# Optimization experiments

Measured on AMD Instinct MI355X. Metric: run time of the kernel, lower is better.

The kernel has to match this reference:

```python
import jax, jax.numpy as jnp
import numpy as np

K0 = 0.7978845608028654  # sqrt(2/pi)
C1 = 0.044715

def _gelu_tanh(x):
    # tanh-approx GELU, matching the Triton kernel's math
    return 0.5 * x * (1.0 + jnp.tanh(K0 * (x + C1 * x * x * x)))

def setup_inputs() -> dict:
    key = jax.random.key(0)
    k1, k2, k3 = jax.random.split(key, 3)
    B, C_in, H, W = 32, 64, 128, 128
    C_out, KH = 128, 3
    x = jax.random.normal(k1, (B, C_in, H, W), dtype=jnp.float32)
    weight = jax.random.normal(k2, (C_out, C_in, KH, KH), dtype=jnp.float32)
    bias = jax.random.normal(k3, (C_out,), dtype=jnp.float32)
    return {"x": x, "weight": weight, "bias": bias}

def reference(x, weight, bias):
    # Valid conv2d, stride 1 (NCHW, OIHW)
    y = jax.lax.conv_general_dilated(
        x, weight,
        window_strides=(1, 1), padding="VALID",
        dimension_numbers=("NCHW", "OIHW", "NCHW"))
    y = y + bias[None, :, None, None]
    y = _gelu_tanh(y)
    # global average pool over spatial dims -> [B, C_out]
    return jnp.mean(y, axis=(2, 3))
```

## Files before the change

kernel.cpp:

```cpp
#include <hip/hip_runtime.h>
#include <cstdint>
#include <cstddef>

#define GK0 0.7978845608028654f
#define GC1 0.044715f

typedef __attribute__((ext_vector_type(8))) short short8;
typedef __attribute__((ext_vector_type(4))) float floatx4;

__device__ __forceinline__ unsigned short f2bf(float f) {
  union { float f; unsigned int u; } v; v.f = f;
  unsigned int r = v.u + 0x7fffu + ((v.u >> 16) & 1u);
  return (unsigned short)(r >> 16);
}

__global__ void k_wt(const float* __restrict__ w, unsigned short* __restrict__ wt,
                     float* __restrict__ out) {
  if (blockIdx.x == 0) {
    for (int i = threadIdx.x; i < 32 * 128; i += 256) out[i] = 0.0f;
  }
  int t = blockIdx.x * 256 + threadIdx.x;
  if (t >= 128 * 64 * 9) return;
  int co = t / 576; int r = t - co * 576; int ci = r / 9; int khw = r - ci * 9;
  wt[(khw * 128 + co) * 64 + ci] = f2bf(w[t]);
}

__global__ __launch_bounds__(256, 2) void k_conv(
    const float* __restrict__ x, const unsigned short* __restrict__ wt,
    const float* __restrict__ bias, float* __restrict__ out) {
  __shared__ unsigned short xs[4 * 66 * 72];
  const int tid = threadIdx.x;
  const int b = blockIdx.z, h0 = blockIdx.y * 2, w0 = blockIdx.x * 64;
  const int lane = tid & 63, wave = tid >> 6;

  {
    const int hi = wave;
    const float* xrow = x + ((size_t)(b * 64) * 128 + (h0 + hi)) * 128 + w0;
    unsigned short* dstrow = xs + (hi * 66 + lane) * 72;
#pragma unroll
    for (int cc = 0; cc < 8; cc++) {
      const float* p = xrow + (size_t)cc * 8 * 16384 + lane;
      short8 v;
#pragma unroll
      for (int j = 0; j < 8; j++) v[j] = (short)f2bf(p[(size_t)j * 16384]);
      *(short8*)(dstrow + cc * 8) = v;
    }
    if (lane < 16) {
      const int e = 64 + (lane & 1), cc = lane >> 1;
      const bool ok = (w0 + e) < 128;
      const float* p = x + ((size_t)(b * 64 + cc * 8) * 128 + (h0 + hi)) * 128 + w0 + e;
      short8 v;
#pragma unroll
      for (int j = 0; j < 8; j++) v[j] = ok ? (short)f2bf(p[(size_t)j * 16384]) : (short)0;
      *(short8*)(xs + (hi * 66 + e) * 72 + cc * 8) = v;
    }
  }
  __syncthreads();

  const int wm = wave & 1, wn = wave >> 1;
  const int m = lane & 15, q = lane >> 4;

  floatx4 acc[4][4];
#pragma unroll
  for (int i = 0; i < 4; i++)
#pragma unroll
    for (int j = 0; j < 4; j++) acc[i][j] = (floatx4){0.f, 0.f, 0.f, 0.f};

  const unsigned short* wbase = wt + ((wm * 64 + m) * 64 + q * 8);
  int bb[4];
#pragma unroll
  for (int nt = 0; nt < 4; nt++) bb[nt] = (wn * 66 + nt * 16 + m) * 72 + q * 8;

  short8 a_cur[4], a_nxt[4];
#pragma unroll
  for (int mt = 0; mt < 4; mt++) a_cur[mt] = *(const short8*)(wbase + mt * 1024);

#pragma unroll
  for (int kk = 0; kk < 18; kk++) {
    const int khw = kk >> 1, cb = (kk & 1) << 5;
    const int kh = khw / 3, kw = khw - kh * 3;
    if (kk < 17) {
      const int khw2 = (kk + 1) >> 1, cb2 = ((kk + 1) & 1) << 5;
      const unsigned short* p = wbase + khw2 * 8192 + cb2;
#pragma unroll
      for (int mt = 0; mt < 4; mt++) a_nxt[mt] = *(const short8*)(p + mt * 1024);
    }
    short8 bf[4];
    const int off = (kh * 66 + kw) * 72 + cb;
#pragma unroll
    for (int nt = 0; nt < 4; nt++) bf[nt] = *(const short8*)(&xs[bb[nt] + off]);
#pragma unroll
    for (int mt = 0; mt < 4; mt++)
#pragma unroll
      for (int nt = 0; nt < 4; nt++)
        acc[mt][nt] = __builtin_amdgcn_mfma_f32_16x16x32_bf16(a_cur[mt], bf[nt], acc[mt][nt], 0, 0, 0);
#pragma unroll
    for (int mt = 0; mt < 4; mt++) a_cur[mt] = a_nxt[mt];
  }

  const float inv_area = 1.0f / (126.0f * 126.0f);
  float* orow = out + b * 128;
#pragma unroll
  for (int mt = 0; mt < 4; mt++) {
#pragma unroll
    for (int r = 0; r < 4; r++) {
      const int co = wm * 64 + mt * 16 + q * 4 + r;
      const float bv = bias[co];
      float s = 0.0f;
#pragma unroll
      for (int nt = 0; nt < 4; nt++) {
        float y = acc[mt][nt][r] + bv;
        float u = GK0 * (y + GC1 * y * y * y);
        float e = __expf(-2.0f * u);
        float g = y * __builtin_amdgcn_rcpf(1.0f + e);
        if (w0 + nt * 16 + m < 126) s += g;
      }
#pragma unroll
      for (int d = 1; d < 16; d <<= 1) s += __shfl_xor(s, d, 64);
      if (m == 0) atomicAdd(&orow[co], s * inv_area);
    }
  }
}

extern "C" void kernel_launch(void* const* d_in, const int* in_sizes, int n_in,
                              void* d_out, int out_size, void* d_ws, size_t ws_size,
                              hipStream_t stream) {
  const float* x    = (const float*)d_in[0];
  const float* w    = (const float*)d_in[1];
  const float* bias = (const float*)d_in[2];
  float* out = (float*)d_out;

  unsigned short* wbuf = (unsigned short*)d_ws;
  if (ws_size < (size_t)9 * 128 * 64 * 2) return;

  k_wt<<<288, 256, 0, stream>>>(w, wbuf, out);
  k_conv<<<dim3(2, 63, 32), 256, 0, stream>>>(x, wbuf, bias, out);
}
```

Before: 400.2 us.

## Process six output rows per block with prefetched input rows and register-accumulated GELU sums

```diff
diff --git a/kernel.cpp b/kernel.cpp
--- a/kernel.cpp
+++ b/kernel.cpp
@@ -6,6 +6,7 @@
 #define GC1 0.044715f
 
 typedef __attribute__((ext_vector_type(8))) short short8;
+typedef __attribute__((ext_vector_type(4))) short short4v;
 typedef __attribute__((ext_vector_type(4))) float floatx4;
 
 __device__ __forceinline__ unsigned short f2bf(float f) {
@@ -28,98 +29,158 @@
 __global__ __launch_bounds__(256, 2) void k_conv(
     const float* __restrict__ x, const unsigned short* __restrict__ wt,
     const float* __restrict__ bias, float* __restrict__ out) {
-  __shared__ unsigned short xs[4 * 66 * 72];
+  __shared__ __align__(16) unsigned short xs[8 * 66 * 72];
   const int tid = threadIdx.x;
-  const int b = blockIdx.z, h0 = blockIdx.y * 2, w0 = blockIdx.x * 64;
+  const int b = blockIdx.z, hbase = blockIdx.y * 6, w0 = blockIdx.x * 64;
   const int lane = tid & 63, wave = tid >> 6;
+  const int wm = wave & 1, wn = wave >> 1;
+  const int m = lane & 15, q = lane >> 4;
+
+  const float* xb = x + (size_t)b * 64 * 16384;
+  const int g = tid >> 4, w4 = tid & 15;
+  const int hci = tid & 63, hrow = tid >> 6;
 
   {
-    const int hi = wave;
-    const float* xrow = x + ((size_t)(b * 64) * 128 + (h0 + hi)) * 128 + w0;
-    unsigned short* dstrow = xs + (hi * 66 + lane) * 72;
+    const float* p0 = xb + (size_t)(4 * g) * 16384 + (size_t)hbase * 128 + w0 + 4 * w4;
+    float4 rv[16];
 #pragma unroll
-    for (int cc = 0; cc < 8; cc++) {
-      const float* p = xrow + (size_t)cc * 8 * 16384 + lane;
-      short8 v;
+    for (int row = 0; row < 4; row++)
 #pragma unroll
-      for (int j = 0; j < 8; j++) v[j] = (short)f2bf(p[(size_t)j * 16384]);
-      *(short8*)(dstrow + cc * 8) = v;
+      for (int c = 0; c < 4; c++)
+        rv[row * 4 + c] = *(const float4*)(p0 + (size_t)c * 16384 + row * 128);
+    float2 hv = make_float2(0.f, 0.f);
+    if (w0 == 0) hv = *(const float2*)(xb + (size_t)hci * 16384 + (size_t)(hbase + hrow) * 128 + 64);
+#pragma unroll
+    for (int row = 0; row < 4; row++) {
+      unsigned short* dr = xs + row * (66 * 72);
+#pragma unroll
+      for (int wj = 0; wj < 4; wj++) {
+        short4v sv;
+#pragma unroll
+        for (int c = 0; c < 4; c++) sv[c] = (short)f2bf(((const float*)&rv[row * 4 + c])[wj]);
+        *(short4v*)(dr + (4 * w4 + wj) * 72 + 4 * g) = sv;
+      }
     }
-    if (lane < 16) {
-      const int e = 64 + (lane & 1), cc = lane >> 1;
-      const bool ok = (w0 + e) < 128;
-      const float* p = x + ((size_t)(b * 64 + cc * 8) * 128 + (h0 + hi)) * 128 + w0 + e;
-      short8 v;
-#pragma unroll
-      for (int j = 0; j < 8; j++) v[j] = ok ? (short)f2bf(p[(size_t)j * 16384]) : (short)0;
-      *(short8*)(xs + (hi * 66 + e) * 72 + cc * 8) = v;
-    }
+    xs[hrow * (66 * 72) + 64 * 72 + hci] = f2bf(hv.x);
+    xs[hrow * (66 * 72) + 65 * 72 + hci] = f2bf(hv.y);
   }
   __syncthreads();
 
-  const int wm = wave & 1, wn = wave >> 1;
-  const int m = lane & 15, q = lane >> 4;
-
-  floatx4 acc[4][4];
+  float bvv[4][4];
 #pragma unroll
-  for (int i = 0; i < 4; i++)
+  for (int mt = 0; mt < 4; mt++)
 #pragma unroll
-    for (int j = 0; j < 4; j++) acc[i][j] = (floatx4){0.f, 0.f, 0.f, 0.f};
+    for (int r2 = 0; r2 < 4; r2++) bvv[mt][r2] = bias[wm * 64 + mt * 16 + q * 4 + r2];
 
   const unsigned short* wbase = wt + ((wm * 64 + m) * 64 + q * 8);
   int bb[4];
 #pragma unroll
-  for (int nt = 0; nt < 4; nt++) bb[nt] = (wn * 66 + nt * 16 + m) * 72 + q * 8;
+  for (int nt = 0; nt < 4; nt++) bb[nt] = (nt * 16 + m) * 72 + q * 8;
 
-  short8 a_cur[4], a_nxt[4];
+  float gsum[4][4];
 #pragma unroll
-  for (int mt = 0; mt < 4; mt++) a_cur[mt] = *(const short8*)(wbase + mt * 1024);
+  for (int i = 0; i < 4; i++)
+#pragma unroll
+    for (int j = 0; j < 4; j++) gsum[i][j] = 0.f;
+
+  for (int t = 0; t < 3; t++) {
+    const bool pre = (t < 2);
+    floatx4 acc[4][4];
+#pragma unroll
+    for (int i = 0; i < 4; i++)
+#pragma unroll
+      for (int j = 0; j < 4; j++) acc[i][j] = (floatx4){0.f, 0.f, 0.f, 0.f};
+
+    short8 a_cur[4], a_nxt[4];
+#pragma unroll
+    for (int mt = 0; mt < 4; mt++) a_cur[mt] = *(const short8*)(wbase + mt * 1024);
+
+    float4 pr[8];
+    float2 ph = make_float2(0.f, 0.f);
 
 #pragma unroll
-  for (int kk = 0; kk < 18; kk++) {
-    const int khw = kk >> 1, cb = (kk & 1) << 5;
-    const int kh = khw / 3, kw = khw - kh * 3;
-    if (kk < 17) {
-      const int khw2 = (kk + 1) >> 1, cb2 = ((kk + 1) & 1) << 5;
-      const unsigned short* p = wbase + khw2 * 8192 + cb2;
+    for (int kk = 0; kk < 18; kk++) {
+      const int khw = kk >> 1, cb = (kk & 1) << 5;
+      const int kh = khw / 3, kw = khw - kh * 3;
+      if (kk < 17) {
+        const int khw2 = (kk + 1) >> 1, cb2 = ((kk + 1) & 1) << 5;
+        const unsigned short* p = wbase + khw2 * 8192 + cb2;
 #pragma unroll
-      for (int mt = 0; mt < 4; mt++) a_nxt[mt] = *(const short8*)(p + mt * 1024);
+        for (int mt = 0; mt < 4; mt++) a_nxt[mt] = *(const short8*)(p + mt * 1024);
+      }
+      short8 bf[4];
+      const int off = ((2 * t + wn + kh) * 66 + kw) * 72 + cb;
+#pragma unroll
+      for (int nt = 0; nt < 4; nt++) bf[nt] = *(const short8*)(&xs[bb[nt] + off]);
+#pragma unroll
+      for (int mt = 0; mt < 4; mt++)
+#pragma unroll
+        for (int nt = 0; nt < 4; nt++)
+          acc[mt][nt] = __builtin_amdgcn_mfma_f32_16x16x32_bf16(a_cur[mt], bf[nt], acc[mt][nt], 0, 0, 0);
+      if (kk == 8 && pre) {
+        const int prow = hbase + 4 + 2 * t;
+        const float* pp = xb + (size_t)(4 * g) * 16384 + (size_t)prow * 128 + w0 + 4 * w4;
+#pragma unroll
+        for (int rr = 0; rr < 2; rr++)
+#pragma unroll
+          for (int c = 0; c < 4; c++)
+            pr[rr * 4 + c] = *(const float4*)(pp + (size_t)c * 16384 + rr * 128);
+        if (w0 == 0 && tid < 128)
+          ph = *(const float2*)(xb + (size_t)hci * 16384 + (size_t)(prow + (hrow & 1)) * 128 + 64);
+      }
+#pragma unroll
+      for (int mt = 0; mt < 4; mt++) a_cur[mt] = a_nxt[mt];
     }
-    short8 bf[4];
-    const int off = (kh * 66 + kw) * 72 + cb;
-#pragma unroll
-    for (int nt = 0; nt < 4; nt++) bf[nt] = *(const short8*)(&xs[bb[nt] + off]);
+
 #pragma unroll
     for (int mt = 0; mt < 4; mt++)
 #pragma unroll
-      for (int nt = 0; nt < 4; nt++)
-        acc[mt][nt] = __builtin_amdgcn_mfma_f32_16x16x32_bf16(a_cur[mt], bf[nt], acc[mt][nt], 0, 0, 0);
+      for (int r2 = 0; r2 < 4; r2++) {
+        float s = 0.f;
 #pragma unroll
-    for (int mt = 0; mt < 4; mt++) a_cur[mt] = a_nxt[mt];
+        for (int nt = 0; nt < 4; nt++) {
+          float y = acc[mt][nt][r2] + bvv[mt][r2];
+          float u = GK0 * (y + GC1 * y * y * y);
+          float e = __expf(-2.0f * u);
+          float gg = y * __builtin_amdgcn_rcpf(1.0f + e);
+          if (w0 + nt * 16 + m < 126) s += gg;
+        }
+        gsum[mt][r2] += s;
+      }
+
+    if (pre) {
+      const int s0 = 4 + 2 * t;
+#pragma unroll
+      for (int rr = 0; rr < 2; rr++) {
+        unsigned short* dr = xs + (s0 + rr) * (66 * 72);
+#pragma unroll
+        for (int wj = 0; wj < 4; wj++) {
+          short4v sv;
+#pragma unroll
+          for (int c = 0; c < 4; c++) sv[c] = (short)f2bf(((const float*)&pr[rr * 4 + c])[wj]);
+          *(short4v*)(dr + (4 * w4 + wj) * 72 + 4 * g) = sv;
+        }
+      }
+      if (tid < 128) {
+        unsigned short* dr = xs + (s0 + (hrow & 1)) * (66 * 72);
+        dr[64 * 72 + hci] = f2bf(ph.x);
+        dr[65 * 72 + hci] = f2bf(ph.y);
+      }
+    }
+    __syncthreads();
   }
 
   const float inv_area = 1.0f / (126.0f * 126.0f);
   float* orow = out + b * 128;
 #pragma unroll
-  for (int mt = 0; mt < 4; mt++) {
+  for (int mt = 0; mt < 4; mt++)
 #pragma unroll
-    for (int r = 0; r < 4; r++) {
-      const int co = wm * 64 + mt * 16 + q * 4 + r;
-      const float bv = bias[co];
-      float s = 0.0f;
-#pragma unroll
-      for (int nt = 0; nt < 4; nt++) {
-        float y = acc[mt][nt][r] + bv;
-        float u = GK0 * (y + GC1 * y * y * y);
-        float e = __expf(-2.0f * u);
-        float g = y * __builtin_amdgcn_rcpf(1.0f + e);
-        if (w0 + nt * 16 + m < 126) s += g;
-      }
+    for (int r2 = 0; r2 < 4; r2++) {
+      float s = gsum[mt][r2];
 #pragma unroll
       for (int d = 1; d < 16; d <<= 1) s += __shfl_xor(s, d, 64);
-      if (m == 0) atomicAdd(&orow[co], s * inv_area);
+      if (m == 0) atomicAdd(&orow[wm * 64 + mt * 16 + q * 4 + r2], s * inv_area);
     }
-  }
 }
 
 extern "C" void kernel_launch(void* const* d_in, const int* in_sizes, int n_in,
@@ -134,5 +195,5 @@
   if (ws_size < (size_t)9 * 128 * 64 * 2) return;
 
   k_wt<<<288, 256, 0, stream>>>(w, wbuf, out);
-  k_conv<<<dim3(2, 63, 32), 256, 0, stream>>>(x, wbuf, bias, out);
+  k_conv<<<dim3(2, 21, 32), 256, 0, stream>>>(x, wbuf, bias, out);
 }
```

Result: slower. 458.0 us (+14.4%).

## Pre-transpose input to NHWC bf16 and stage tiles with global_load_lds

Applied to the files above, without the earlier changes.

```diff
diff --git a/kernel.cpp b/kernel.cpp
--- a/kernel.cpp
+++ b/kernel.cpp
@@ -14,6 +14,12 @@
   return (unsigned short)(r >> 16);
 }
 
+__device__ __forceinline__ void gl_lds16(const unsigned short* g, unsigned short* l) {
+  __builtin_amdgcn_global_load_lds(
+      (const __attribute__((address_space(1))) unsigned int*)g,
+      (__attribute__((address_space(3))) unsigned int*)l, 16, 0, 0);
+}
+
 __global__ void k_wt(const float* __restrict__ w, unsigned short* __restrict__ wt,
                      float* __restrict__ out) {
   if (blockIdx.x == 0) {
@@ -25,39 +31,44 @@
   wt[(khw * 128 + co) * 64 + ci] = f2bf(w[t]);
 }
 
-__global__ __launch_bounds__(256, 2) void k_conv(
-    const float* __restrict__ x, const unsigned short* __restrict__ wt,
-    const float* __restrict__ bias, float* __restrict__ out) {
-  __shared__ unsigned short xs[4 * 66 * 72];
-  const int tid = threadIdx.x;
-  const int b = blockIdx.z, h0 = blockIdx.y * 2, w0 = blockIdx.x * 64;
-  const int lane = tid & 63, wave = tid >> 6;
+__global__ __launch_bounds__(256) void k_xt(const float* __restrict__ x,
+                                            unsigned short* __restrict__ xb) {
+  __shared__ float tile[64 * 132];
+  const int tid = threadIdx.x, lane = tid & 63, wv = tid >> 6;
+  const int b = blockIdx.y, h0 = blockIdx.x * 4;
+  const int w4 = lane & 31, cih = lane >> 5;
 
-  {
-    const int hi = wave;
-    const float* xrow = x + ((size_t)(b * 64) * 128 + (h0 + hi)) * 128 + w0;
-    unsigned short* dstrow = xs + (hi * 66 + lane) * 72;
+  for (int r = 0; r < 4; r++) {
+    const int h = h0 + r;
 #pragma unroll
-    for (int cc = 0; cc < 8; cc++) {
-      const float* p = xrow + (size_t)cc * 8 * 16384 + lane;
+    for (int j = 0; j < 8; j++) {
+      const int ci = wv * 16 + 2 * j + cih;
+      float4 f = *(const float4*)(x + ((size_t)(b * 64 + ci) * 128 + h) * 128 + 4 * w4);
+      *(float4*)&tile[ci * 132 + 4 * w4] = f;
+    }
+    __syncthreads();
+    unsigned short* orow = xb + ((size_t)b * 128 + h) * 8192;
+    const int oct = tid & 7, wlo = tid >> 3;
+#pragma unroll
+    for (int it = 0; it < 4; it++) {
+      const int w = wlo + 32 * it;
       short8 v;
 #pragma unroll
-      for (int j = 0; j < 8; j++) v[j] = (short)f2bf(p[(size_t)j * 16384]);
-      *(short8*)(dstrow + cc * 8) = v;
+      for (int j = 0; j < 8; j++) v[j] = (short)f2bf(tile[(8 * oct + j) * 132 + w]);
+      *(short8*)(orow + w * 64 + oct * 8) = v;
     }
-    if (lane < 16) {
-      const int e = 64 + (lane & 1), cc = lane >> 1;
-      const bool ok = (w0 + e) < 128;
-      const float* p = x + ((size_t)(b * 64 + cc * 8) * 128 + (h0 + hi)) * 128 + w0 + e;
-      short8 v;
-#pragma unroll
-      for (int j = 0; j < 8; j++) v[j] = ok ? (short)f2bf(p[(size_t)j * 16384]) : (short)0;
-      *(short8*)(xs + (hi * 66 + e) * 72 + cc * 8) = v;
-    }
+    __syncthreads();
   }
-  __syncthreads();
+}
 
-  const int wm = wave & 1, wn = wave >> 1;
+__global__ __launch_bounds__(256, 3) void k_conv(
+    const unsigned short* __restrict__ xb, const unsigned short* __restrict__ wt,
+    const float* __restrict__ bias, float* __restrict__ out) {
+  __shared__ __align__(16) unsigned short As[8192];
+  __shared__ __align__(16) unsigned short Bs[8192];
+  const int tid = threadIdx.x, lane = tid & 63, wv = tid >> 6;
+  const int w0 = blockIdx.x * 64, h0 = blockIdx.y * 2, b = blockIdx.z;
+  const int wm = wv & 1, wn = wv >> 1;
   const int m = lane & 15, q = lane >> 4;
 
   floatx4 acc[4][4];
@@ -66,50 +77,53 @@
 #pragma unroll
     for (int j = 0; j < 4; j++) acc[i][j] = (floatx4){0.f, 0.f, 0.f, 0.f};
 
-  const unsigned short* wbase = wt + ((wm * 64 + m) * 64 + q * 8);
-  int bb[4];
-#pragma unroll
-  for (int nt = 0; nt < 4; nt++) bb[nt] = (wn * 66 + nt * 16 + m) * 72 + q * 8;
-
-  short8 a_cur[4], a_nxt[4];
-#pragma unroll
-  for (int mt = 0; mt < 4; mt++) a_cur[mt] = *(const short8*)(wbase + mt * 1024);
+  const unsigned short* xbb = xb + (size_t)b * 128 * 8192;
+  const int rh = wv >> 1, cc0 = (wv & 1) * 4;
 
 #pragma unroll
-  for (int kk = 0; kk < 18; kk++) {
-    const int khw = kk >> 1, cb = (kk & 1) << 5;
-    const int kh = khw / 3, kw = khw - kh * 3;
-    if (kk < 17) {
-      const int khw2 = (kk + 1) >> 1, cb2 = ((kk + 1) & 1) << 5;
-      const unsigned short* p = wbase + khw2 * 8192 + cb2;
+  for (int khw = 0; khw < 9; khw++) {
+    const int kh = khw / 3, kw = khw - 3 * kh;
+    const unsigned short* ag = wt + khw * 8192 + wv * 2048 + lane * 8;
+    unsigned short* al = As + wv * 2048;
 #pragma unroll
-      for (int mt = 0; mt < 4; mt++) a_nxt[mt] = *(const short8*)(p + mt * 1024);
-    }
-    short8 bf[4];
-    const int off = (kh * 66 + kw) * 72 + cb;
+    for (int i = 0; i < 4; i++) gl_lds16(ag + i * 512, al + i * 512);
+    const unsigned short* bg =
+        xbb + ((size_t)(h0 + rh + kh) * 128 + w0 + kw) * 64 + cc0 * 512 + lane * 8;
+    unsigned short* bl = Bs + (rh * 8 + cc0) * 512;
 #pragma unroll
-    for (int nt = 0; nt < 4; nt++) bf[nt] = *(const short8*)(&xs[bb[nt] + off]);
+    for (int i = 0; i < 4; i++) gl_lds16(bg + i * 512, bl + i * 512);
+    __syncthreads();
+
 #pragma unroll
-    for (int mt = 0; mt < 4; mt++)
+    for (int half = 0; half < 2; half++) {
+      short8 a[4], bf[4];
+#pragma unroll
+      for (int mt = 0; mt < 4; mt++)
+        a[mt] = *(const short8*)&As[(wm * 64 + mt * 16 + m) * 64 + half * 32 + q * 8];
 #pragma unroll
       for (int nt = 0; nt < 4; nt++)
-        acc[mt][nt] = __builtin_amdgcn_mfma_f32_16x16x32_bf16(a_cur[mt], bf[nt], acc[mt][nt], 0, 0, 0);
+        bf[nt] = *(const short8*)&Bs[(wn * 64 + nt * 16 + m) * 64 + half * 32 + q * 8];
 #pragma unroll
-    for (int mt = 0; mt < 4; mt++) a_cur[mt] = a_nxt[mt];
+      for (int mt = 0; mt < 4; mt++)
+#pragma unroll
+        for (int nt = 0; nt < 4; nt++)
+          acc[mt][nt] = __builtin_amdgcn_mfma_f32_16x16x32_bf16(a[mt], bf[nt], acc[mt][nt], 0, 0, 0);
+    }
+    __syncthreads();
   }
 
   const float inv_area = 1.0f / (126.0f * 126.0f);
   float* orow = out + b * 128;
 #pragma unroll
-  for (int mt = 0; mt < 4; mt++) {
+  for (int mt = 0; mt < 4; mt++)
 #pragma unroll
-    for (int r = 0; r < 4; r++) {
-      const int co = wm * 64 + mt * 16 + q * 4 + r;
+    for (int r2 = 0; r2 < 4; r2++) {
+      const int co = wm * 64 + mt * 16 + q * 4 + r2;
       const float bv = bias[co];
-      float s = 0.0f;
+      float s = 0.f;
 #pragma unroll
       for (int nt = 0; nt < 4; nt++) {
-        float y = acc[mt][nt][r] + bv;
+        float y = acc[mt][nt][r2] + bv;
         float u = GK0 * (y + GC1 * y * y * y);
         float e = __expf(-2.0f * u);
         float g = y * __builtin_amdgcn_rcpf(1.0f + e);
@@ -119,7 +133,6 @@
       for (int d = 1; d < 16; d <<= 1) s += __shfl_xor(s, d, 64);
       if (m == 0) atomicAdd(&orow[co], s * inv_area);
     }
-  }
 }
 
 extern "C" void kernel_launch(void* const* d_in, const int* in_sizes, int n_in,
@@ -130,9 +143,12 @@
   const float* bias = (const float*)d_in[2];
   float* out = (float*)d_out;
 
-  unsigned short* wbuf = (unsigned short*)d_ws;
-  if (ws_size < (size_t)9 * 128 * 64 * 2) return;
+  const size_t xb_elems = (size_t)32 * 128 * 8192;
+  unsigned short* xbuf = (unsigned short*)d_ws;
+  unsigned short* wbuf = xbuf + xb_elems + 2048;
+  if (ws_size < xb_elems * 2 + 4096 + (size_t)9 * 128 * 64 * 2) return;
 
   k_wt<<<288, 256, 0, stream>>>(w, wbuf, out);
-  k_conv<<<dim3(2, 63, 32), 256, 0, stream>>>(x, wbuf, bias, out);
+  k_xt<<<dim3(32, 32), 256, 0, stream>>>(x, xbuf);
+  k_conv<<<dim3(2, 63, 32), 256, 0, stream>>>(xbuf, wbuf, bias, out);
 }
```

Measured after the change: 380.6 us. 1.05x faster.
